# Performance work log

Measured on AMD Instinct MI355X. Metric: run time of the kernel, lower is better.

## Reference

```python
import jax, jax.numpy as jnp
import numpy as np

N_NODES = 50000
N_EDGES = 800000
NFEAT, NHID, NCLASS = 512, 256, 64


def _glorot(key, fan_in, fan_out):
    # mimics kipf-style uniform init: U(-1/sqrt(fan_out), 1/sqrt(fan_out))
    stdv = 1.0 / np.sqrt(fan_out)
    return jax.random.uniform(key, (fan_in, fan_out), jnp.float32, -stdv, stdv)


def setup_inputs() -> dict:
    key = jax.random.key(0)
    ks = jax.random.split(key, 8)
    x = jax.random.normal(ks[0], (N_NODES, NFEAT), jnp.float32)
    edge_src = jax.random.randint(ks[1], (N_EDGES,), 0, N_NODES, jnp.int32)
    edge_dst = jax.random.randint(ks[2], (N_EDGES,), 0, N_NODES, jnp.int32)
    edge_weight = jax.random.uniform(ks[3], (N_EDGES,), jnp.float32)
    W1 = _glorot(ks[4], NFEAT, NHID)
    b1 = jax.random.uniform(ks[5], (NHID,), jnp.float32, -1.0 / np.sqrt(NHID), 1.0 / np.sqrt(NHID))
    W2 = _glorot(ks[6], NHID, NCLASS)
    b2 = jax.random.uniform(ks[7], (NCLASS,), jnp.float32, -1.0 / np.sqrt(NCLASS), 1.0 / np.sqrt(NCLASS))
    return {"x": x, "W1": W1, "b1": b1, "W2": W2, "b2": b2,
            "edge_weight": edge_weight, "edge_src": edge_src, "edge_dst": edge_dst}


def _spmm(edge_src, edge_dst, edge_weight, support):
    # adj @ support with adj given as COO edge list: out[d] += w * support[s]
    msgs = support[edge_src] * edge_weight[:, None]  # [E, F]
    return jax.ops.segment_sum(msgs, edge_dst, num_segments=N_NODES)


def reference(x, W1, b1, W2, b2, edge_weight, edge_src, edge_dst):
    # layer 1: GraphConvolution -> ReLU (dropout identity in eval mode)
    h = _spmm(edge_src, edge_dst, edge_weight, x @ W1) + b1
    h = jax.nn.relu(h)
    # layer 2: GraphConvolution -> log_softmax over classes
    logits = _spmm(edge_src, edge_dst, edge_weight, h @ W2) + b2
    return jax.nn.log_softmax(logits, axis=1)
```

## Files before the change

kernel.cpp:

```cpp
#include <hip/hip_runtime.h>
#include <cstdint>


typedef unsigned short u16;
typedef unsigned int u32;
typedef __attribute__((ext_vector_type(8))) short bf16x8;
typedef __attribute__((ext_vector_type(4))) float f32x4;

#define N_NODES 50000
#define N_EDGES 800000
#define NFEAT 512
#define NHID 256
#define NCLASS 64
#define CSTRIDE 64
#define DEGS 16

#define SB  391
#define GB1 782
#define PW1B 512
#define PW2B 64
#define DEGZB 196
#define FNB 3125

__device__ __forceinline__ float bf2f(u16 h) {
    union { u32 u; float f; } c; c.u = ((u32)h) << 16; return c.f;
}
__device__ __forceinline__ u16 f2bf(float f) {
    union { float f; u32 u; } c; c.f = f;
    u32 u = c.u;
    return (u16)((u + 0x7fffu + ((u >> 16) & 1u)) >> 16);
}
__device__ __forceinline__ u32 pk2(float a, float b) {
    return (u32)f2bf(a) | ((u32)f2bf(b) << 16);
}

__device__ __forceinline__ void async16(const void* g, void* l) {
    __builtin_amdgcn_global_load_lds(
        (const __attribute__((address_space(1))) void*)(uintptr_t)g,
        (__attribute__((address_space(3))) void*)(uintptr_t)l, 16, 0, 0);
}


__global__ __launch_bounds__(256) void prep0_kernel(
    const float* __restrict__ W1, u16* __restrict__ W1T,
    const float* __restrict__ W2, u16* __restrict__ W2T,
    int* __restrict__ deg) {
    int b = blockIdx.x;
    if (b < PW1B) {
        int idx = b * 256 + threadIdx.x;
        int n = idx >> 9, k = idx & 511;
        W1T[idx] = f2bf(W1[(size_t)k * NHID + n]);
    } else if (b < PW1B + PW2B) {
        int idx = (b - PW1B) * 256 + threadIdx.x;
        int n = idx >> 8, k = idx & 255;
        W2T[idx] = f2bf(W2[(size_t)k * NCLASS + n]);
    } else {
        int base = (b - PW1B - PW2B) * 4096 + threadIdx.x * 16;
        if (base < N_NODES * DEGS) {
            int4 z = make_int4(0, 0, 0, 0);
            int4* p = (int4*)(deg + base);
            p[0] = z; p[1] = z; p[2] = z; p[3] = z;
        }
    }
}


template <int MT, int NT, int WCOLS, int K, bool ACVT>
__device__ __forceinline__ void gemm_body(const void* __restrict__ Av,
                                          const u16* __restrict__ BT,
                                          u16* __restrict__ C, int M,
                                          int bid, u16* lds) {
    constexpr int WROWS = 4 / WCOLS;
    constexpr int RT = MT / (16 * WROWS);
    constexpr int CT = NT / (16 * WCOLS);
    u16* As = lds;
    u16* Bs = lds + MT * 64;

    const int tid  = threadIdx.x;
    const int wv   = tid >> 6, lane = tid & 63;
    const int lm   = lane & 15, quad = lane >> 4;
    const int wrow = wv / WCOLS, wcol = wv % WCOLS;
    const int m0   = bid * MT;
    const int co0 = ((0 * 4 + quad) ^ (lm & 7)) * 8;
    const int co1 = ((1 * 4 + quad) ^ (lm & 7)) * 8;

    f32x4 acc[RT][CT];
    #pragma unroll
    for (int r = 0; r < RT; ++r)
        #pragma unroll
        for (int c = 0; c < CT; ++c) acc[r][c] = (f32x4){0.f, 0.f, 0.f, 0.f};

    for (int k0 = 0; k0 < K; k0 += 64) {
        if constexpr (ACVT) {
            static_assert(MT == 64, "ACVT staging assumes MT==64 (16 elems/thread)");
            const float* Af = (const float*)Av;
            int row = tid >> 2, ko = (tid & 3) * 16;
            int gr = m0 + row; if (gr > M - 1) gr = M - 1;
            const float4* gp = (const float4*)(Af + (size_t)gr * K + k0 + ko);
            float4 f0 = gp[0], f1 = gp[1], f2 = gp[2], f3 = gp[3];
            #pragma unroll
            for (int i = 0; i < NT / 32; ++i) {
                int c = i * 256 + tid;
                int n = c >> 3, kb = c & 7;
                async16(BT + (size_t)n * K + k0 + ((kb ^ (n & 7)) * 8), Bs + c * 8);
            }
            u32 p[8] = {pk2(f0.x, f0.y), pk2(f0.z, f0.w), pk2(f1.x, f1.y), pk2(f1.z, f1.w),
                        pk2(f2.x, f2.y), pk2(f2.z, f2.w), pk2(f3.x, f3.y), pk2(f3.z, f3.w)};
            int ch0 = (2 * (tid & 3))     ^ (row & 7);
            int ch1 = (2 * (tid & 3) + 1) ^ (row & 7);
            *(int4*)(As + row * 64 + ch0 * 8) = *(int4*)&p[0];
            *(int4*)(As + row * 64 + ch1 * 8) = *(int4*)&p[4];
        } else {
            const u16* A = (const u16*)Av;
            #pragma unroll
            for (int i = 0; i < NT / 32; ++i) {
                int c = i * 256 + tid;
                int n = c >> 3, kb = c & 7;
                async16(BT + (size_t)n * K + k0 + ((kb ^ (n & 7)) * 8), Bs + c * 8);
            }
            #pragma unroll
            for (int i = 0; i < MT / 32; ++i) {
                int c = i * 256 + tid;
                int row = c >> 3, kb = c & 7;
                int gr = m0 + row; if (gr > M - 1) gr = M - 1;
                async16(A + (size_t)gr * K + k0 + ((kb ^ (row & 7)) * 8), As + c * 8);
            }
        }
        __syncthreads();

        #pragma unroll
        for (int kk = 0; kk < 2; ++kk) {
            const int co = kk ? co1 : co0;
            bf16x8 af[RT], bfv[CT];
            #pragma unroll
            for (int rt = 0; rt < RT; ++rt) {
                int row = wrow * (RT * 16) + rt * 16 + lm;
                af[rt] = *(const bf16x8*)(As + row * 64 + co);
            }
            #pragma unroll
            for (int ct = 0; ct < CT; ++ct) {
                int n = wcol * CT * 16 + ct * 16 + lm;
                bfv[ct] = *(const bf16x8*)(Bs + n * 64 + co);
            }
            #pragma unroll
            for (int rt = 0; rt < RT; ++rt)
                #pragma unroll
                for (int ct = 0; ct < CT; ++ct)
                    acc[rt][ct] = __builtin_amdgcn_mfma_f32_16x16x32_bf16(
                        af[rt], bfv[ct], acc[rt][ct], 0, 0, 0);
        }
        __syncthreads();
    }

    #pragma unroll
    for (int rt = 0; rt < RT; ++rt)
        #pragma unroll
        for (int ct = 0; ct < CT; ++ct) {
            int col = wcol * CT * 16 + ct * 16 + lm;
            #pragma unroll
            for (int r = 0; r < 4; ++r) {
                int row = wrow * (RT * 16) + rt * 16 + quad * 4 + r;
                lds[row * NT + col] = f2bf(acc[rt][ct][r]);
            }
        }
    __syncthreads();
    constexpr int NC = MT * NT / 2048;
    #pragma unroll
    for (int i = 0; i < NC; ++i) {
        int c = i * 256 + tid;
        int row = (c * 8) / NT;
        if (m0 + row < M)
            *(int4*)(C + (size_t)m0 * NT + c * 8) = *(const int4*)(lds + c * 8);
    }
}


__global__ __launch_bounds__(256) void gemm1_scatter_kernel(
    const float* __restrict__ x, const u16* __restrict__ W1T, u16* __restrict__ S1,
    const int* __restrict__ esrc, const int* __restrict__ edst,
    const float* __restrict__ ew, int* __restrict__ deg, u32* __restrict__ csr) {
    __shared__ __align__(16) u16 lds[(64 + 256) * 64];
    int b = blockIdx.x;
    if (b < SB) {
        int e0 = (b * 256 + threadIdx.x) * 8;
        if (e0 < N_EDGES) {
            int4 d0 = *(const int4*)(edst + e0),  d1 = *(const int4*)(edst + e0 + 4);
            int4 s0 = *(const int4*)(esrc + e0),  s1 = *(const int4*)(esrc + e0 + 4);
            float4 w0 = *(const float4*)(ew + e0), w1 = *(const float4*)(ew + e0 + 4);
            int d[8] = {d0.x, d0.y, d0.z, d0.w, d1.x, d1.y, d1.z, d1.w};
            int s[8] = {s0.x, s0.y, s0.z, s0.w, s1.x, s1.y, s1.z, s1.w};
            float w[8] = {w0.x, w0.y, w0.z, w0.w, w1.x, w1.y, w1.z, w1.w};
            int r[8];
            #pragma unroll
            for (int i = 0; i < 8; ++i)
                r[i] = atomicAdd(&deg[d[i] * DEGS], 1);
            #pragma unroll
            for (int i = 0; i < 8; ++i)
                if (r[i] < CSTRIDE)
                    csr[(size_t)d[i] * CSTRIDE + r[i]] = (u32)s[i] | ((u32)f2bf(w[i]) << 16);
        }
    } else {
        gemm_body<64, 256, 4, NFEAT, true>(x, W1T, S1, N_NODES, b - SB, lds);
    }
}


__global__ __launch_bounds__(256) void spmm1_gemm2_kernel(
    const u16* __restrict__ S, const int* __restrict__ deg,
    const u32* __restrict__ csr, const float* __restrict__ bias1,
    const u16* __restrict__ W2T, u16* __restrict__ S2) {
    __shared__ __align__(16) u16 Hs[16 * 256];
    __shared__ __align__(16) u16 Bs[64 * 64];

    const int tid  = threadIdx.x;
    const int wv   = tid >> 6, lane = tid & 63;
    const int lm   = lane & 15, quad = lane >> 4;
    const int b    = blockIdx.x;

    float4 bv = *(const float4*)(bias1 + lane * 4);

    #pragma unroll
    for (int it = 0; it < 4; ++it) {
        int lrow = wv * 4 + it;
        int node = __builtin_amdgcn_readfirstlane(b * 16 + lrow);
        int beg = node * CSTRIDE;
        int end = beg + deg[node * DEGS];
        float a0 = 0.f, a1 = 0.f, a2 = 0.f, a3 = 0.f;
        int j = beg;
        for (; j + 8 <= end; j += 8) {
            u32 e[8];
            #pragma unroll
            for (int i = 0; i < 8; ++i) e[i] = csr[j + i];
            ushort4 v[8];
            #pragma unroll
            for (int i = 0; i < 8; ++i)
                v[i] = *(const ushort4*)(S + (size_t)(e[i] & 0xFFFFu) * NHID + lane * 4);
            #pragma unroll
            for (int i = 0; i < 8; ++i) {
                float w = bf2f((u16)(e[i] >> 16));
                a0 += w * bf2f(v[i].x); a1 += w * bf2f(v[i].y);
                a2 += w * bf2f(v[i].z); a3 += w * bf2f(v[i].w);
            }
        }
        for (; j < end; ++j) {
            u32 e0 = csr[j];
            float w = bf2f((u16)(e0 >> 16));
            ushort4 v0 = *(const ushort4*)(S + (size_t)(e0 & 0xFFFFu) * NHID + lane * 4);
            a0 += w * bf2f(v0.x); a1 += w * bf2f(v0.y);
            a2 += w * bf2f(v0.z); a3 += w * bf2f(v0.w);
        }
        a0 = fmaxf(a0 + bv.x, 0.f);
        a1 = fmaxf(a1 + bv.y, 0.f);
        a2 = fmaxf(a2 + bv.z, 0.f);
        a3 = fmaxf(a3 + bv.w, 0.f);
        int ch = (lane >> 1) ^ (lrow & 7);
        u32* dp = (u32*)(Hs + lrow * 256 + ch * 8 + (lane & 1) * 4);
        dp[0] = pk2(a0, a1);
        dp[1] = pk2(a2, a3);
    }
    __syncthreads();

    f32x4 acc = (f32x4){0.f, 0.f, 0.f, 0.f};
    for (int k0 = 0; k0 < NHID; k0 += 64) {
        #pragma unroll
        for (int i = 0; i < 2; ++i) {
            int c = i * 256 + tid;
            int n = c >> 3, kb = c & 7;
            async16(W2T + (size_t)n * NHID + k0 + ((kb ^ (n & 7)) * 8), Bs + c * 8);
        }
        __syncthreads();
        #pragma unroll
        for (int kk = 0; kk < 2; ++kk) {
            int ca = ((k0 >> 3) + kk * 4 + quad) ^ (lm & 7);
            bf16x8 af = *(const bf16x8*)(Hs + lm * 256 + ca * 8);
            int n = wv * 16 + lm;
            int cb = (kk * 4 + quad) ^ (n & 7);
            bf16x8 bf = *(const bf16x8*)(Bs + n * 64 + cb * 8);
            acc = __builtin_amdgcn_mfma_f32_16x16x32_bf16(af, bf, acc, 0, 0, 0);
        }
        __syncthreads();
    }

    #pragma unroll
    for (int r = 0; r < 4; ++r) {
        int row = quad * 4 + r;
        Hs[row * 64 + wv * 16 + lm] = f2bf(acc[r]);
    }
    __syncthreads();
    *(ushort4*)(S2 + (size_t)b * 1024 + tid * 4) = *(const ushort4*)(Hs + tid * 4);
}


__global__ __launch_bounds__(256) void spmm_bias_lsm_kernel(
    const u16* __restrict__ S, const int* __restrict__ deg,
    const u32* __restrict__ csr, const float* __restrict__ bias,
    float* __restrict__ out, int n) {
    int node = blockIdx.x * 4 + (threadIdx.x >> 6);
    if (node >= n) return;
    node = __builtin_amdgcn_readfirstlane(node);
    int lane = threadIdx.x & 63;
    int beg = node * CSTRIDE;
    int end = beg + deg[node * DEGS];
    float acc = 0.f;
    int j = beg;
    for (; j + 8 <= end; j += 8) {
        u32 e[8];
        #pragma unroll
        for (int i = 0; i < 8; ++i) e[i] = csr[j + i];
        u16 v[8];
        #pragma unroll
        for (int i = 0; i < 8; ++i)
            v[i] = S[(size_t)(e[i] & 0xFFFFu) * NCLASS + lane];
        #pragma unroll
        for (int i = 0; i < 8; ++i)
            acc += bf2f((u16)(e[i] >> 16)) * bf2f(v[i]);
    }
    for (; j < end; ++j) {
        u32 e0 = csr[j];
        acc += bf2f((u16)(e0 >> 16)) * bf2f(S[(size_t)(e0 & 0xFFFFu) * NCLASS + lane]);
    }

    float x = acc + bias[lane];
    float m = x;
    #pragma unroll
    for (int off = 32; off > 0; off >>= 1) m = fmaxf(m, __shfl_xor(m, off));
    float e = expf(x - m);
    float ssum = e;
    #pragma unroll
    for (int off = 32; off > 0; off >>= 1) ssum += __shfl_xor(ssum, off);
    out[(size_t)node * NCLASS + lane] = x - m - logf(ssum);
}


extern "C" void kernel_launch(void* const* d_in, const int* in_sizes, int n_in,
                              void* d_out, int out_size, void* d_ws, size_t ws_size,
                              hipStream_t stream) {
    const float* x  = (const float*)d_in[0];
    const float* W1 = (const float*)d_in[1];
    const float* b1 = (const float*)d_in[2];
    const float* W2 = (const float*)d_in[3];
    const float* b2 = (const float*)d_in[4];
    const float* ew = (const float*)d_in[5];
    const int* esrc = (const int*)d_in[6];
    const int* edst = (const int*)d_in[7];
    float* out = (float*)d_out;

    char* ws = (char*)d_ws;
    size_t off = 0;
    auto take = [&](size_t bytes) -> void* {
        off = (off + 255) & ~(size_t)255;
        void* p = ws + off;
        off += bytes;
        return p;
    };
    u16* S1  = (u16*)take((size_t)N_NODES * NHID * 2);
    u16* S2  = (u16*)take((size_t)N_NODES * NCLASS * 2);
    u16* W1T = (u16*)take((size_t)NHID * NFEAT * 2);
    u16* W2T = (u16*)take((size_t)NCLASS * NHID * 2);
    int* deg = (int*)take((size_t)N_NODES * DEGS * 4);
    u32* csr = (u32*)take((size_t)N_NODES * CSTRIDE * 4);
    (void)ws_size; (void)in_sizes; (void)n_in; (void)out_size;

    prep0_kernel<<<PW1B + PW2B + DEGZB, 256, 0, stream>>>(W1, W1T, W2, W2T, deg);
    gemm1_scatter_kernel<<<SB + GB1, 256, 0, stream>>>(x, W1T, S1, esrc, edst, ew,
                                                       deg, csr);
    spmm1_gemm2_kernel<<<FNB, 256, 0, stream>>>(S1, deg, csr, b1, W2T, S2);
    spmm_bias_lsm_kernel<<<(N_NODES + 3) / 4, 256, 0, stream>>>(
        S2, deg, csr, b2, out, N_NODES);
}
```

Before: 298.8 us.

## Build CSR via two-pass bucketed scatter with LDS atomics instead of global atomics

Replaces the per-edge global atomicAdd on padded degree counters with a two-level bucket sort. Edges are first binned into 196 buckets of 256 destination nodes using block-local LDS counters and one global atomic per bucket per block. A new kernel then sorts each bucket into the fixed-stride CSR with LDS atomics and writes compact degrees. This cuts global atomic contention and the zeroing of the padded degree array, but adds a kernel launch, an intermediate 8-byte-per-edge buffer, and a fixed per-bucket capacity that could overflow if degrees are skewed.

New measurement: 288.9 us. 1.03x faster.

```diff
diff --git a/kernel.cpp b/kernel.cpp
--- a/kernel.cpp
+++ b/kernel.cpp
@@ -4,6 +4,7 @@
 
 typedef unsigned short u16;
 typedef unsigned int u32;
+typedef unsigned long long u64;
 typedef __attribute__((ext_vector_type(8))) short bf16x8;
 typedef __attribute__((ext_vector_type(4))) float f32x4;
 
@@ -13,13 +14,13 @@
 #define NHID 256
 #define NCLASS 64
 #define CSTRIDE 64
-#define DEGS 16
-
-#define SB  391
+
+#define NBUCK 196
+#define BCAP 5120
+#define SCB 391
 #define GB1 782
 #define PW1B 512
 #define PW2B 64
-#define DEGZB 196
 #define FNB 3125
 
 __device__ __forceinline__ float bf2f(u16 h) {
@@ -44,7 +45,7 @@
 __global__ __launch_bounds__(256) void prep0_kernel(
     const float* __restrict__ W1, u16* __restrict__ W1T,
     const float* __restrict__ W2, u16* __restrict__ W2T,
-    int* __restrict__ deg) {
+    int* __restrict__ fill) {
     int b = blockIdx.x;
     if (b < PW1B) {
         int idx = b * 256 + threadIdx.x;
@@ -55,12 +56,7 @@
         int n = idx >> 8, k = idx & 255;
         W2T[idx] = f2bf(W2[(size_t)k * NCLASS + n]);
     } else {
-        int base = (b - PW1B - PW2B) * 4096 + threadIdx.x * 16;
-        if (base < N_NODES * DEGS) {
-            int4 z = make_int4(0, 0, 0, 0);
-            int4* p = (int4*)(deg + base);
-            p[0] = z; p[1] = z; p[2] = z; p[3] = z;
-        }
+        if (threadIdx.x < NBUCK) fill[threadIdx.x] = 0;
     }
 }
 
@@ -178,29 +174,74 @@
 __global__ __launch_bounds__(256) void gemm1_scatter_kernel(
     const float* __restrict__ x, const u16* __restrict__ W1T, u16* __restrict__ S1,
     const int* __restrict__ esrc, const int* __restrict__ edst,
-    const float* __restrict__ ew, int* __restrict__ deg, u32* __restrict__ csr) {
+    const float* __restrict__ ew, int* __restrict__ fill, u64* __restrict__ region) {
     __shared__ __align__(16) u16 lds[(64 + 256) * 64];
     int b = blockIdx.x;
-    if (b < SB) {
-        int e0 = (b * 256 + threadIdx.x) * 8;
-        if (e0 < N_EDGES) {
+    int tid = threadIdx.x;
+    if (b < SCB) {
+        int* cnt  = (int*)lds;
+        int* base = cnt + NBUCK;
+        if (tid < NBUCK) cnt[tid] = 0;
+        __syncthreads();
+        int e0 = b * 2048 + tid * 8;
+        int d[8], s[8], rk[8];
+        float w[8];
+        bool act = (e0 < N_EDGES);
+        if (act) {
             int4 d0 = *(const int4*)(edst + e0),  d1 = *(const int4*)(edst + e0 + 4);
             int4 s0 = *(const int4*)(esrc + e0),  s1 = *(const int4*)(esrc + e0 + 4);
             float4 w0 = *(const float4*)(ew + e0), w1 = *(const float4*)(ew + e0 + 4);
-            int d[8] = {d0.x, d0.y, d0.z, d0.w, d1.x, d1.y, d1.z, d1.w};
-            int s[8] = {s0.x, s0.y, s0.z, s0.w, s1.x, s1.y, s1.z, s1.w};
-            float w[8] = {w0.x, w0.y, w0.z, w0.w, w1.x, w1.y, w1.z, w1.w};
-            int r[8];
+            d[0]=d0.x; d[1]=d0.y; d[2]=d0.z; d[3]=d0.w;
+            d[4]=d1.x; d[5]=d1.y; d[6]=d1.z; d[7]=d1.w;
+            s[0]=s0.x; s[1]=s0.y; s[2]=s0.z; s[3]=s0.w;
+            s[4]=s1.x; s[5]=s1.y; s[6]=s1.z; s[7]=s1.w;
+            w[0]=w0.x; w[1]=w0.y; w[2]=w0.z; w[3]=w0.w;
+            w[4]=w1.x; w[5]=w1.y; w[6]=w1.z; w[7]=w1.w;
             #pragma unroll
             for (int i = 0; i < 8; ++i)
-                r[i] = atomicAdd(&deg[d[i] * DEGS], 1);
-            #pragma unroll
-            for (int i = 0; i < 8; ++i)
-                if (r[i] < CSTRIDE)
-                    csr[(size_t)d[i] * CSTRIDE + r[i]] = (u32)s[i] | ((u32)f2bf(w[i]) << 16);
+                rk[i] = atomicAdd(&cnt[d[i] >> 8], 1);
+        }
+        __syncthreads();
+        if (tid < NBUCK) base[tid] = atomicAdd(&fill[tid], cnt[tid]);
+        __syncthreads();
+        if (act) {
+            #pragma unroll
+            for (int i = 0; i < 8; ++i) {
+                int g = d[i] >> 8;
+                int pos = base[g] + rk[i];
+                if (pos < BCAP) {
+                    u64 en = ((u64)(d[i] & 255) << 32) |
+                             (u64)((u32)s[i] | ((u32)f2bf(w[i]) << 16));
+                    region[(size_t)g * BCAP + pos] = en;
+                }
+            }
         }
     } else {
-        gemm_body<64, 256, 4, NFEAT, true>(x, W1T, S1, N_NODES, b - SB, lds);
+        gemm_body<64, 256, 4, NFEAT, true>(x, W1T, S1, N_NODES, b - SCB, lds);
+    }
+}
+
+
+__global__ __launch_bounds__(256) void csr_sort_kernel(
+    const u64* __restrict__ region, const int* __restrict__ fill,
+    u32* __restrict__ csr, int* __restrict__ deg) {
+    __shared__ int cnt2[256];
+    int b = blockIdx.x, tid = threadIdx.x;
+    cnt2[tid] = 0;
+    __syncthreads();
+    int Eb = fill[b]; if (Eb > BCAP) Eb = BCAP;
+    for (int i = tid; i < Eb; i += 256) {
+        u64 en = region[(size_t)b * BCAP + i];
+        int dlo = (int)(en >> 32) & 255;
+        int r = atomicAdd(&cnt2[dlo], 1);
+        if (r < CSTRIDE)
+            csr[(size_t)(b * 256 + dlo) * CSTRIDE + r] = (u32)en;
+    }
+    __syncthreads();
+    int node = b * 256 + tid;
+    if (node < N_NODES) {
+        int dg = cnt2[tid]; if (dg > CSTRIDE) dg = CSTRIDE;
+        deg[node] = dg;
     }
 }
 
@@ -224,7 +265,7 @@
         int lrow = wv * 4 + it;
         int node = __builtin_amdgcn_readfirstlane(b * 16 + lrow);
         int beg = node * CSTRIDE;
-        int end = beg + deg[node * DEGS];
+        int end = beg + deg[node];
         float a0 = 0.f, a1 = 0.f, a2 = 0.f, a3 = 0.f;
         int j = beg;
         for (; j + 8 <= end; j += 8) {
@@ -300,7 +341,7 @@
     node = __builtin_amdgcn_readfirstlane(node);
     int lane = threadIdx.x & 63;
     int beg = node * CSTRIDE;
-    int end = beg + deg[node * DEGS];
+    int end = beg + deg[node];
     float acc = 0.f;
     int j = beg;
     for (; j + 8 <= end; j += 8) {
@@ -353,17 +394,20 @@
         off += bytes;
         return p;
     };
-    u16* S1  = (u16*)take((size_t)N_NODES * NHID * 2);
-    u16* S2  = (u16*)take((size_t)N_NODES * NCLASS * 2);
-    u16* W1T = (u16*)take((size_t)NHID * NFEAT * 2);
-    u16* W2T = (u16*)take((size_t)NCLASS * NHID * 2);
-    int* deg = (int*)take((size_t)N_NODES * DEGS * 4);
-    u32* csr = (u32*)take((size_t)N_NODES * CSTRIDE * 4);
+    u16* S1   = (u16*)take((size_t)N_NODES * NHID * 2);
+    u16* S2   = (u16*)take((size_t)N_NODES * NCLASS * 2);
+    u16* W1T  = (u16*)take((size_t)NHID * NFEAT * 2);
+    u16* W2T  = (u16*)take((size_t)NCLASS * NHID * 2);
+    int* deg  = (int*)take((size_t)N_NODES * 4);
+    u32* csr  = (u32*)take((size_t)N_NODES * CSTRIDE * 4);
+    int* fill = (int*)take((size_t)NBUCK * 4);
+    u64* region = (u64*)take((size_t)NBUCK * BCAP * 8);
     (void)ws_size; (void)in_sizes; (void)n_in; (void)out_size;
 
-    prep0_kernel<<<PW1B + PW2B + DEGZB, 256, 0, stream>>>(W1, W1T, W2, W2T, deg);
-    gemm1_scatter_kernel<<<SB + GB1, 256, 0, stream>>>(x, W1T, S1, esrc, edst, ew,
-                                                       deg, csr);
+    prep0_kernel<<<PW1B + PW2B + 1, 256, 0, stream>>>(W1, W1T, W2, W2T, fill);
+    gemm1_scatter_kernel<<<SCB + GB1, 256, 0, stream>>>(x, W1T, S1, esrc, edst, ew,
+                                                        fill, region);
+    csr_sort_kernel<<<NBUCK, 256, 0, stream>>>(region, fill, csr, deg);
     spmm1_gemm2_kernel<<<FNB, 256, 0, stream>>>(S1, deg, csr, b1, W2T, S2);
     spmm_bias_lsm_kernel<<<(N_NODES + 3) / 4, 256, 0, stream>>>(
         S2, deg, csr, b2, out, N_NODES);
```
